# Performance work log

Measured on AMD Instinct MI355X. Metric: run time of the kernel, lower is better.

Reference implementation:

```python
import jax, jax.numpy as jnp
import numpy as np

B, L, D, H = 2, 2048, 1024, 16
DH = D // H
LN_EPS = 1e-5


def setup_inputs() -> dict:
    key = jax.random.key(0)
    ks = jax.random.split(key, 6)
    s = 1.0 / np.sqrt(D)
    return {
        "x": jax.random.normal(ks[0], (B, L, D), dtype=jnp.float32),
        "market_info": jax.random.uniform(ks[1], (B, 8), dtype=jnp.float32),
        "in_proj_w": jax.random.normal(ks[2], (3 * D, D), dtype=jnp.float32) * s,
        "in_proj_b": jnp.zeros((3 * D,), dtype=jnp.float32),
        "out_proj_w": jax.random.normal(ks[3], (D, D), dtype=jnp.float32) * s,
        "out_proj_b": jnp.zeros((D,), dtype=jnp.float32),
        "ln_gamma": jnp.ones((D,), dtype=jnp.float32),
        "ln_beta": jnp.zeros((D,), dtype=jnp.float32),
    }


def reference(x, market_info, in_proj_w, in_proj_b, out_proj_w, out_proj_b, ln_gamma, ln_beta):
    # fused QKV projection (torch nn.MultiheadAttention in_proj)
    qkv = jnp.einsum("bld,ed->ble", x, in_proj_w) + in_proj_b  # (B,L,3D)
    q, k, v = jnp.split(qkv, 3, axis=-1)
    q = q.reshape(B, L, H, DH)
    k = k.reshape(B, L, H, DH)
    v = v.reshape(B, L, H, DH)
    scale = 1.0 / jnp.sqrt(jnp.asarray(DH, dtype=x.dtype))
    scores = jnp.einsum("blhd,bmhd->bhlm", q, k) * scale  # (B,H,L,L)
    # market mask: per-batch volatility scalar added to every score
    vol = market_info[:, 0][:, None, None, None]  # (B,1,1,1)
    attn = jax.nn.softmax(scores + vol, axis=-1)
    ctx = jnp.einsum("bhlm,bmhd->blhd", attn, v).reshape(B, L, D)
    attended = jnp.einsum("bld,ed->ble", ctx, out_proj_w) + out_proj_b
    # residual + LayerNorm (dropout=0 / eval)
    y = x + attended
    mu = jnp.mean(y, axis=-1, keepdims=True)
    var = jnp.mean(jnp.square(y - mu), axis=-1, keepdims=True)
    return (y - mu) * jax.lax.rsqrt(var + LN_EPS) * ln_gamma + ln_beta
```

## Files before the change

### kernel.cpp

```cpp
#include <hip/hip_runtime.h>
#include <math.h>

#define B_  2
#define L_  2048
#define D_  1024
#define H_  16
#define DH_ 64
#define E3D 3072
#define LN_EPS 1e-5f

typedef unsigned short u16;
typedef __attribute__((ext_vector_type(8))) short bf16x8;
typedef __attribute__((ext_vector_type(4))) float f32x4;

__device__ inline unsigned pack2(float lo, float hi) {
    unsigned a = __builtin_bit_cast(unsigned, lo) + 0x8000u;
    unsigned b = __builtin_bit_cast(unsigned, hi) + 0x8000u;
    return __builtin_amdgcn_perm(b, a, 0x07060302);
}
__device__ inline float bf2f(u16 v) {
    return __builtin_bit_cast(float, (unsigned)v << 16);
}
__device__ inline void async16(const void* g, void* l) {
    __builtin_amdgcn_global_load_lds(
        (const __attribute__((address_space(1))) unsigned*)g,
        (__attribute__((address_space(3))) unsigned*)l, 16, 0, 0);
}

__global__ __launch_bounds__(256) void cvt_bf16(
    const float* __restrict__ src, u16* __restrict__ dst, int n)
{
    const int i = (blockIdx.x * 256 + threadIdx.x) * 8;
    if (i >= n) return;
    float4 v0 = *(const float4*)(src + i);
    float4 v1 = *(const float4*)(src + i + 4);
    uint4 w;
    w.x = pack2(v0.x, v0.y); w.y = pack2(v0.z, v0.w);
    w.z = pack2(v1.x, v1.y); w.w = pack2(v1.z, v1.w);
    *(uint4*)(dst + i) = w;
}

__global__ __launch_bounds__(256) void gemm_bf16(
    const u16* __restrict__ A, const u16* __restrict__ W,
    const float* __restrict__ bias, const float* __restrict__ resid,
    float* __restrict__ outF, u16* __restrict__ outB,
    int M, int N, int K, int qlimit)
{
    __shared__ __align__(16) u16 As[128 * 32];
    __shared__ __align__(16) u16 Ws[128 * 32];

    const int t    = threadIdx.x;
    const int wave = t >> 6;
    const int lane = t & 63;
    const int a    = lane & 15;
    const int g    = lane >> 4;
    const int row0 = blockIdx.y * 128;
    const int col0 = blockIdx.x * 128;

    const int srow = wave * 32 + (lane >> 2);
    const int sseg = (lane & 3) * 8;
    const u16* Ag = A + (size_t)(row0 + srow) * K + sseg;
    const u16* Wg = W + (size_t)(col0 + srow) * K + sseg;
    u16* AsW = &As[wave * 32 * 32];
    u16* WsW = &Ws[wave * 32 * 32];

    f32x4 acc[4][4];
    #pragma unroll
    for (int i = 0; i < 4; ++i)
        #pragma unroll
        for (int j = 0; j < 4; ++j)
            acc[i][j] = (f32x4){0.f, 0.f, 0.f, 0.f};

    const int ar = (wave & 1) * 64;
    const int wc = (wave >> 1) * 64;

    for (int kt = 0; kt < K; kt += 32) {
        __syncthreads();
        async16(Ag + kt,                  AsW);
        async16(Ag + (size_t)16 * K + kt, AsW + 16 * 32);
        async16(Wg + kt,                  WsW);
        async16(Wg + (size_t)16 * K + kt, WsW + 16 * 32);
        __syncthreads();

        bf16x8 af[4], wf[4];
        #pragma unroll
        for (int i = 0; i < 4; ++i)
            af[i] = *(const bf16x8*)&As[(ar + i * 16 + a) * 32 + g * 8];
        #pragma unroll
        for (int j = 0; j < 4; ++j)
            wf[j] = *(const bf16x8*)&Ws[(wc + j * 16 + a) * 32 + g * 8];
        #pragma unroll
        for (int i = 0; i < 4; ++i)
            #pragma unroll
            for (int j = 0; j < 4; ++j)
                acc[i][j] = __builtin_amdgcn_mfma_f32_16x16x32_bf16(
                    wf[j], af[i], acc[i][j], 0, 0, 0);
    }

    if (outB != nullptr) {
        const float s = (col0 < qlimit) ? 0.125f : 1.0f;
        #pragma unroll
        for (int j = 0; j < 4; ++j) {
            const int cb = col0 + wc + j * 16 + g * 4;
            const float4 bj = *(const float4*)(bias + cb);
            #pragma unroll
            for (int i = 0; i < 4; ++i) {
                const int row = row0 + ar + i * 16 + a;
                uint2 w;
                w.x = pack2((acc[i][j][0] + bj.x) * s, (acc[i][j][1] + bj.y) * s);
                w.y = pack2((acc[i][j][2] + bj.z) * s, (acc[i][j][3] + bj.w) * s);
                *(uint2*)&outB[(size_t)row * N + cb] = w;
            }
        }
    } else {
        #pragma unroll
        for (int j = 0; j < 4; ++j) {
            const int cb = col0 + wc + j * 16 + g * 4;
            const float4 bj = *(const float4*)(bias + cb);
            #pragma unroll
            for (int i = 0; i < 4; ++i) {
                const int row = row0 + ar + i * 16 + a;
                const size_t idx = (size_t)row * N + cb;
                const float4 xr = *(const float4*)(resid + idx);
                float4 o;
                o.x = acc[i][j][0] + bj.x + xr.x;
                o.y = acc[i][j][1] + bj.y + xr.y;
                o.z = acc[i][j][2] + bj.z + xr.z;
                o.w = acc[i][j][3] + bj.w + xr.w;
                *(float4*)&outF[idx] = o;
            }
        }
    }
}

__global__ __launch_bounds__(256) void attn_mfma(
    const u16* __restrict__ qkv, u16* __restrict__ Oun, float* __restrict__ lbuf)
{
    const int bid  = blockIdx.x;
    const int half = bid >> 9;
    const int rest = bid & 511;
    const int qt   = rest & 15;
    const int bh   = rest >> 4;
    const int h    = bh & 15;
    const int b    = bh >> 4;
    const int qb0  = qt * 128;

    const int t    = threadIdx.x;
    const int wave = t >> 6;
    const int lane = t & 63;
    const int a    = lane & 15;
    const int g    = lane >> 4;

    __shared__ __align__(16) u16 Kt[64 * 72];
    __shared__ __align__(16) u16 VtT[64 * 72];
    __shared__ __align__(16) u16 Pl[4 * 2 * 16 * 72];

    bf16x8 qf[2][2];
    #pragma unroll
    for (int q2 = 0; q2 < 2; ++q2) {
        const u16* qrow = qkv + (size_t)(b * L_ + qb0 + wave * 32 + q2 * 16 + a) * E3D
                        + h * DH_;
        #pragma unroll
        for (int c = 0; c < 2; ++c)
            qf[q2][c] = *(const bf16x8*)(qrow + c * 32 + g * 8);
    }

    f32x4 o[2][4];
    #pragma unroll
    for (int q2 = 0; q2 < 2; ++q2)
        #pragma unroll
        for (int dt = 0; dt < 4; ++dt)
            o[q2][dt] = (f32x4){0.f, 0.f, 0.f, 0.f};
    float psum[2] = {0.f, 0.f};

    const int krow = t >> 2;
    const int kseg = (t & 3) * 16;
    const int vu   = t >> 3;
    const int vc8  = (t & 7) * 8;
    const int vj0  = t & 7;

    const int k_lo = half * (L_ / 2);
    for (int k0 = k_lo; k0 < k_lo + L_ / 2; k0 += 64) {
        __syncthreads();

        {
            const u16* kr = qkv + (size_t)(b * L_ + k0 + krow) * E3D + D_ + h * DH_ + kseg;
            uint4 x0 = *(const uint4*)kr;
            uint4 x1 = *(const uint4*)(kr + 8);
            *(uint4*)&Kt[krow * 72 + kseg]     = x0;
            *(uint4*)&Kt[krow * 72 + kseg + 8] = x1;
        }
        {
            const u16* vr = qkv + (size_t)(b * L_ + k0 + 2 * vu) * E3D + 2 * D_ + h * DH_ + vc8;
            uint4 va = *(const uint4*)vr;
            uint4 vb = *(const uint4*)(vr + E3D);
            const unsigned av[4] = {va.x, va.y, va.z, va.w};
            const unsigned bv[4] = {vb.x, vb.y, vb.z, vb.w};
            unsigned* Vw = (unsigned*)VtT;
            #pragma unroll
            for (int i = 0; i < 8; ++i) {
                const int j = (i + vj0) & 7;
                const unsigned xa = av[j >> 1], xb = bv[j >> 1];
                const unsigned v = (j & 1) ? ((xa >> 16) | (xb & 0xffff0000u))
                                           : ((xa & 0xffffu) | (xb << 16));
                Vw[(vc8 + j) * 36 + vu] = v;
            }
        }
        __syncthreads();

        f32x4 s[2][4];
        #pragma unroll
        for (int q2 = 0; q2 < 2; ++q2)
            #pragma unroll
            for (int kt = 0; kt < 4; ++kt)
                s[q2][kt] = (f32x4){0.f, 0.f, 0.f, 0.f};
        #pragma unroll
        for (int kt = 0; kt < 4; ++kt) {
            bf16x8 kf0 = *(const bf16x8*)&Kt[(kt * 16 + a) * 72 + g * 8];
            bf16x8 kf1 = *(const bf16x8*)&Kt[(kt * 16 + a) * 72 + 32 + g * 8];
            #pragma unroll
            for (int q2 = 0; q2 < 2; ++q2) {
                s[q2][kt] = __builtin_amdgcn_mfma_f32_16x16x32_bf16(kf0, qf[q2][0], s[q2][kt], 0, 0, 0);
                s[q2][kt] = __builtin_amdgcn_mfma_f32_16x16x32_bf16(kf1, qf[q2][1], s[q2][kt], 0, 0, 0);
            }
        }

        #pragma unroll
        for (int q2 = 0; q2 < 2; ++q2) {
            float ps = 0.f;
            #pragma unroll
            for (int kt = 0; kt < 4; ++kt)
                #pragma unroll
                for (int r = 0; r < 4; ++r) {
                    const float p = __expf(s[q2][kt][r]);
                    s[q2][kt][r] = p;
                    ps += p;
                }
            psum[q2] += ps;
            unsigned* Pw = (unsigned*)&Pl[(wave * 2 + q2) * (16 * 72)];
            #pragma unroll
            for (int kt = 0; kt < 4; ++kt) {
                Pw[a * 36 + kt * 8 + g * 2 + 0] = pack2(s[q2][kt][0], s[q2][kt][1]);
                Pw[a * 36 + kt * 8 + g * 2 + 1] = pack2(s[q2][kt][2], s[q2][kt][3]);
            }
        }

        #pragma unroll
        for (int c = 0; c < 2; ++c) {
            bf16x8 pf[2];
            #pragma unroll
            for (int q2 = 0; q2 < 2; ++q2)
                pf[q2] = *(const bf16x8*)&Pl[(wave * 2 + q2) * (16 * 72) + a * 72 + c * 32 + g * 8];
            #pragma unroll
            for (int dt = 0; dt < 4; ++dt) {
                bf16x8 vf = *(const bf16x8*)&VtT[(dt * 16 + a) * 72 + c * 32 + g * 8];
                #pragma unroll
                for (int q2 = 0; q2 < 2; ++q2)
                    o[q2][dt] = __builtin_amdgcn_mfma_f32_16x16x32_bf16(vf, pf[q2], o[q2][dt], 0, 0, 0);
            }
        }
    }

    #pragma unroll
    for (int q2 = 0; q2 < 2; ++q2) {
        const int qrow = qb0 + wave * 32 + q2 * 16 + a;
        const size_t row = (size_t)(b * L_ + qrow);
        float ps = psum[q2];
        ps += __shfl_xor(ps, 16);
        ps += __shfl_xor(ps, 32);
        if (g == 0)
            lbuf[(size_t)half * 65536 + row * 16 + h] = ps;
        u16* cp = Oun + (size_t)half * 4096 * 1024 + row * D_ + h * DH_;
        #pragma unroll
        for (int dt = 0; dt < 4; ++dt) {
            uint2 w;
            w.x = pack2(o[q2][dt][0], o[q2][dt][1]);
            w.y = pack2(o[q2][dt][2], o[q2][dt][3]);
            *(uint2*)&cp[dt * 16 + g * 4] = w;
        }
    }
}

__global__ __launch_bounds__(256) void attn_merge(
    const u16* __restrict__ Oun, const float* __restrict__ lbuf,
    u16* __restrict__ ctx)
{
    const int row = blockIdx.x;
    const int t   = threadIdx.x;
    const int col = t * 4;
    const int h   = col >> 6;
    const float inv = 1.f / (lbuf[(size_t)row * 16 + h] +
                             lbuf[(size_t)65536 + row * 16 + h]);
    const size_t base = (size_t)row * D_ + col;
    uint2 w0 = *(const uint2*)&Oun[base];
    uint2 w1 = *(const uint2*)&Oun[(size_t)4096 * 1024 + base];
    float f0 = (bf2f((u16)(w0.x & 0xffff)) + bf2f((u16)(w1.x & 0xffff))) * inv;
    float f1 = (bf2f((u16)(w0.x >> 16))    + bf2f((u16)(w1.x >> 16)))    * inv;
    float f2 = (bf2f((u16)(w0.y & 0xffff)) + bf2f((u16)(w1.y & 0xffff))) * inv;
    float f3 = (bf2f((u16)(w0.y >> 16))    + bf2f((u16)(w1.y >> 16)))    * inv;
    uint2 w;
    w.x = pack2(f0, f1);
    w.y = pack2(f2, f3);
    *(uint2*)&ctx[base] = w;
}

__global__ __launch_bounds__(256) void ln_rows(
    const float* __restrict__ y, const float* __restrict__ gamma,
    const float* __restrict__ beta, float* __restrict__ out)
{
    const int row = blockIdx.x;
    const int t = threadIdx.x;
    const float* yr = y + (size_t)row * D_;

    float4 v = *(const float4*)(yr + t * 4);
    float s  = v.x + v.y + v.z + v.w;
    float s2 = v.x * v.x + v.y * v.y + v.z * v.z + v.w * v.w;
    #pragma unroll
    for (int off = 32; off > 0; off >>= 1) {
        s  += __shfl_down(s, off);
        s2 += __shfl_down(s2, off);
    }
    __shared__ float red[4], red2[4];
    const int wid = t >> 6, lid = t & 63;
    if (lid == 0) { red[wid] = s; red2[wid] = s2; }
    __syncthreads();
    if (t == 0) {
        float aa = 0.f, b2 = 0.f;
        #pragma unroll
        for (int i = 0; i < 4; ++i) { aa += red[i]; b2 += red2[i]; }
        red[0] = aa; red2[0] = b2;
    }
    __syncthreads();
    const float mu   = red[0] * (1.f / D_);
    const float var  = red2[0] * (1.f / D_) - mu * mu;
    const float rstd = rsqrtf(var + LN_EPS);

    float4 gm = *(const float4*)(gamma + t * 4);
    float4 bt = *(const float4*)(beta + t * 4);
    float4 oo;
    oo.x = (v.x - mu) * rstd * gm.x + bt.x;
    oo.y = (v.y - mu) * rstd * gm.y + bt.y;
    oo.z = (v.z - mu) * rstd * gm.z + bt.z;
    oo.w = (v.w - mu) * rstd * gm.w + bt.w;
    *(float4*)(out + (size_t)row * D_ + t * 4) = oo;
}

extern "C" void kernel_launch(void* const* d_in, const int* in_sizes, int n_in,
                              void* d_out, int out_size, void* d_ws, size_t ws_size,
                              hipStream_t stream)
{
    const float* x      = (const float*)d_in[0];
    const float* in_w   = (const float*)d_in[2];
    const float* in_b   = (const float*)d_in[3];
    const float* out_w  = (const float*)d_in[4];
    const float* out_b  = (const float*)d_in[5];
    const float* gamma  = (const float*)d_in[6];
    const float* beta   = (const float*)d_in[7];
    float* out = (float*)d_out;

    char* ws   = (char*)d_ws;
    u16*  qkvb = (u16*)ws;
    u16*  Oun  = (u16*)(ws + 25165824);
    u16*  ctxb = (u16*)(ws + 41943040);
    u16*  xb   = (u16*)(ws + 50331648);
    float* lb  = (float*)(ws + 50331648);
    u16*  iwb  = (u16*)(ws + 58720256);
    u16*  owb  = (u16*)(ws + 65011712);
    float* y   = (float*)ws;

    dim3 blk(256);
    cvt_bf16<<<dim3(4096 * 1024 / 2048), blk, 0, stream>>>(x, xb, 4096 * 1024);
    cvt_bf16<<<dim3(3072 * 1024 / 2048), blk, 0, stream>>>(in_w, iwb, 3072 * 1024);
    cvt_bf16<<<dim3(1024 * 1024 / 2048), blk, 0, stream>>>(out_w, owb, 1024 * 1024);

    gemm_bf16<<<dim3(E3D / 128, (B_ * L_) / 128), blk, 0, stream>>>(
        xb, iwb, in_b, nullptr, nullptr, qkvb, B_ * L_, E3D, D_, D_);

    attn_mfma<<<dim3(2 * B_ * H_ * (L_ / 128)), blk, 0, stream>>>(qkvb, Oun, lb);
    attn_merge<<<dim3(B_ * L_), blk, 0, stream>>>(Oun, lb, ctxb);

    gemm_bf16<<<dim3(D_ / 128, (B_ * L_) / 128), blk, 0, stream>>>(
        ctxb, owb, out_b, x, y, nullptr, B_ * L_, D_, D_, 0);

    ln_rows<<<dim3(B_ * L_), blk, 0, stream>>>(y, gamma, beta, out);
}
```

Before: 255.8 us.

## Fuse conversion launches, load K directly to registers, use exp2 softmax

Merges the three fp32-to-bf16 conversion kernels into one launch. Attention now loads K fragments straight from global memory into registers, with the V loads issued before the barrier, and drops the K shared-memory tile. The log2(e) factor is folded into the Q scale so softmax can use the native exp2, and P stores are widened to 64-bit. The aim is to cut launch overhead, LDS traffic and exp cost. The trade-off is more register pressure and uncoalesced strided K loads from global memory.

Result: slower. 276.2 us (+8.0%).

```diff
diff --git a/kernel.cpp b/kernel.cpp
--- a/kernel.cpp
+++ b/kernel.cpp
@@ -27,11 +27,19 @@
         (__attribute__((address_space(3))) unsigned*)l, 16, 0, 0);
 }
 
-__global__ __launch_bounds__(256) void cvt_bf16(
-    const float* __restrict__ src, u16* __restrict__ dst, int n)
-{
-    const int i = (blockIdx.x * 256 + threadIdx.x) * 8;
-    if (i >= n) return;
+#define QSCALE (0.125f * 1.44269504088896f)
+
+__global__ __launch_bounds__(256) void cvt_all(
+    const float* __restrict__ x, const float* __restrict__ iw,
+    const float* __restrict__ ow, u16* __restrict__ xb,
+    u16* __restrict__ iwb, u16* __restrict__ owb)
+{
+    const int bid = blockIdx.x;
+    const float* src; u16* dst; int base;
+    if (bid < 2048)      { src = x;  dst = xb;  base = bid * 2048; }
+    else if (bid < 3584) { src = iw; dst = iwb; base = (bid - 2048) * 2048; }
+    else                 { src = ow; dst = owb; base = (bid - 3584) * 2048; }
+    const int i = base + threadIdx.x * 8;
     float4 v0 = *(const float4*)(src + i);
     float4 v1 = *(const float4*)(src + i + 4);
     uint4 w;
@@ -98,7 +106,7 @@
     }
 
     if (outB != nullptr) {
-        const float s = (col0 < qlimit) ? 0.125f : 1.0f;
+        const float s = (col0 < qlimit) ? QSCALE : 1.0f;
         #pragma unroll
         for (int j = 0; j < 4; ++j) {
             const int cb = col0 + wc + j * 16 + g * 4;
@@ -151,7 +159,6 @@
     const int a    = lane & 15;
     const int g    = lane >> 4;
 
-    __shared__ __align__(16) u16 Kt[64 * 72];
     __shared__ __align__(16) u16 VtT[64 * 72];
     __shared__ __align__(16) u16 Pl[4 * 2 * 16 * 72];
 
@@ -173,27 +180,27 @@
             o[q2][dt] = (f32x4){0.f, 0.f, 0.f, 0.f};
     float psum[2] = {0.f, 0.f};
 
-    const int krow = t >> 2;
-    const int kseg = (t & 3) * 16;
+    const u16* kfb = qkv + (size_t)(b * L_) * E3D + D_ + h * DH_ + g * 8;
     const int vu   = t >> 3;
     const int vc8  = (t & 7) * 8;
     const int vj0  = t & 7;
 
     const int k_lo = half * (L_ / 2);
     for (int k0 = k_lo; k0 < k_lo + L_ / 2; k0 += 64) {
+        bf16x8 kf[4][2];
+        #pragma unroll
+        for (int kt = 0; kt < 4; ++kt) {
+            const u16* kp = kfb + (size_t)(k0 + kt * 16 + a) * E3D;
+            kf[kt][0] = *(const bf16x8*)kp;
+            kf[kt][1] = *(const bf16x8*)(kp + 32);
+        }
+        const u16* vr = qkv + (size_t)(b * L_ + k0 + 2 * vu) * E3D + 2 * D_ + h * DH_ + vc8;
+        uint4 va = *(const uint4*)vr;
+        uint4 vb = *(const uint4*)(vr + E3D);
+
         __syncthreads();
 
         {
-            const u16* kr = qkv + (size_t)(b * L_ + k0 + krow) * E3D + D_ + h * DH_ + kseg;
-            uint4 x0 = *(const uint4*)kr;
-            uint4 x1 = *(const uint4*)(kr + 8);
-            *(uint4*)&Kt[krow * 72 + kseg]     = x0;
-            *(uint4*)&Kt[krow * 72 + kseg + 8] = x1;
-        }
-        {
-            const u16* vr = qkv + (size_t)(b * L_ + k0 + 2 * vu) * E3D + 2 * D_ + h * DH_ + vc8;
-            uint4 va = *(const uint4*)vr;
-            uint4 vb = *(const uint4*)(vr + E3D);
             const unsigned av[4] = {va.x, va.y, va.z, va.w};
             const unsigned bv[4] = {vb.x, vb.y, vb.z, vb.w};
             unsigned* Vw = (unsigned*)VtT;
@@ -215,15 +222,12 @@
             for (int kt = 0; kt < 4; ++kt)
                 s[q2][kt] = (f32x4){0.f, 0.f, 0.f, 0.f};
         #pragma unroll
-        for (int kt = 0; kt < 4; ++kt) {
-            bf16x8 kf0 = *(const bf16x8*)&Kt[(kt * 16 + a) * 72 + g * 8];
-            bf16x8 kf1 = *(const bf16x8*)&Kt[(kt * 16 + a) * 72 + 32 + g * 8];
+        for (int kt = 0; kt < 4; ++kt)
             #pragma unroll
             for (int q2 = 0; q2 < 2; ++q2) {
-                s[q2][kt] = __builtin_amdgcn_mfma_f32_16x16x32_bf16(kf0, qf[q2][0], s[q2][kt], 0, 0, 0);
-                s[q2][kt] = __builtin_amdgcn_mfma_f32_16x16x32_bf16(kf1, qf[q2][1], s[q2][kt], 0, 0, 0);
-            }
-        }
+                s[q2][kt] = __builtin_amdgcn_mfma_f32_16x16x32_bf16(kf[kt][0], qf[q2][0], s[q2][kt], 0, 0, 0);
+                s[q2][kt] = __builtin_amdgcn_mfma_f32_16x16x32_bf16(kf[kt][1], qf[q2][1], s[q2][kt], 0, 0, 0);
+            }
 
         #pragma unroll
         for (int q2 = 0; q2 < 2; ++q2) {
@@ -232,7 +236,7 @@
             for (int kt = 0; kt < 4; ++kt)
                 #pragma unroll
                 for (int r = 0; r < 4; ++r) {
-                    const float p = __expf(s[q2][kt][r]);
+                    const float p = __builtin_amdgcn_exp2f(s[q2][kt][r]);
                     s[q2][kt][r] = p;
                     ps += p;
                 }
@@ -240,8 +244,10 @@
             unsigned* Pw = (unsigned*)&Pl[(wave * 2 + q2) * (16 * 72)];
             #pragma unroll
             for (int kt = 0; kt < 4; ++kt) {
-                Pw[a * 36 + kt * 8 + g * 2 + 0] = pack2(s[q2][kt][0], s[q2][kt][1]);
-                Pw[a * 36 + kt * 8 + g * 2 + 1] = pack2(s[q2][kt][2], s[q2][kt][3]);
+                uint2 w;
+                w.x = pack2(s[q2][kt][0], s[q2][kt][1]);
+                w.y = pack2(s[q2][kt][2], s[q2][kt][3]);
+                *(uint2*)&Pw[a * 36 + kt * 8 + g * 2] = w;
             }
         }
 
@@ -369,9 +375,7 @@
     float* y   = (float*)ws;
 
     dim3 blk(256);
-    cvt_bf16<<<dim3(4096 * 1024 / 2048), blk, 0, stream>>>(x, xb, 4096 * 1024);
-    cvt_bf16<<<dim3(3072 * 1024 / 2048), blk, 0, stream>>>(in_w, iwb, 3072 * 1024);
-    cvt_bf16<<<dim3(1024 * 1024 / 2048), blk, 0, stream>>>(out_w, owb, 1024 * 1024);
+    cvt_all<<<dim3(4096), blk, 0, stream>>>(x, in_w, out_w, xb, iwb, owb);
 
     gemm_bf16<<<dim3(E3D / 128, (B_ * L_) / 128), blk, 0, stream>>>(
         xb, iwb, in_b, nullptr, nullptr, qkvb, B_ * L_, E3D, D_, D_);
```
